# Kernel tuning notes

Measured on AMD Instinct MI355X. Metric: run time of the kernel, lower is better.

Reference implementation:

```python
import jax, jax.numpy as jnp
import numpy as np

B, H, W, DIM = 1, 256, 256, 192
HEADS = 6
K, DIL = 7, 2            # NAttention kernel / dilation
WS, DF = 8, 2            # stripe window size, anchor down factor
AWS = WS // DF           # anchor window size (4)
N1, N2 = WS * WS, AWS * AWS
L = H * W
CPB_HID = 512


def _nbr(size, k, d):
    # 1D neighborhood-attention neighbor indices with dilation (edge-clamped)
    i = np.arange(size); g = i % d; p = i // d
    gsize = size // d  # d divides size
    start = np.clip(p - k // 2, 0, gsize - k)
    nbr_p = start[:, None] + np.arange(k)[None, :]
    nbr = g[:, None] + d * nbr_p                    # absolute key index
    rb = nbr_p - p[:, None] + (k - 1)               # rpb index in [0, 2k-2]
    return nbr.astype(np.int32), rb.astype(np.int32)

NBR_H, RB_H = _nbr(H, K, DIL)
NBR_W, RB_W = _nbr(W, K, DIL)


def _na_attention(q, k, v, rpb):
    # q,k,v: (B, heads, H, W, hd); rpb: (heads, 2K-1, 2K-1)
    bias = rpb[:, RB_H, :]                          # (heads,H,K,2K-1)
    bias = jnp.take(bias, RB_W, axis=3)             # (heads,H,K,W,K)
    bias = jnp.transpose(bias, (0, 1, 3, 2, 4))     # (heads,H,W,K,K)
    logits = []
    for ki in range(K):
        kh = jnp.take(k, NBR_H[:, ki], axis=2)
        for kj in range(K):
            khw = jnp.take(kh, NBR_W[:, kj], axis=3)
            logits.append(jnp.einsum('bnhwc,bnhwc->bnhw', q, khw))
    a = jnp.stack(logits, axis=-1).reshape(*q.shape[:4], K, K) + bias[None]
    a = jax.nn.softmax(a.reshape(*q.shape[:4], K * K), axis=-1).reshape(*q.shape[:4], K, K)
    out = jnp.zeros_like(q)
    for ki in range(K):
        vh = jnp.take(v, NBR_H[:, ki], axis=2)
        for kj in range(K):
            vhw = jnp.take(vh, NBR_W[:, kj], axis=3)
            out = out + a[..., ki, kj, None] * vhw
    return out

na_attention = jax.checkpoint(_na_attention)


def window_partition(x, ws):
    b, h, w, c = x.shape
    x = x.reshape(b, h // ws, ws, w // ws, ws, c)
    return jnp.transpose(x, (0, 1, 3, 2, 4, 5)).reshape(-1, ws * ws, c)


def window_reverse(x, ws, h, w):
    c = x.shape[-1]
    b = x.shape[0] // ((h // ws) * (w // ws))
    x = x.reshape(b, h // ws, w // ws, ws, ws, c)
    return jnp.transpose(x, (0, 1, 3, 2, 4, 5)).reshape(b, h, w, c)


def _l2n(x):
    n = jnp.linalg.norm(x, axis=-1, keepdims=True)
    return x / jnp.maximum(n, 1e-12)


def _affine(attn, table, index, ls, w1, b1, w2):
    # attn: (Bw, heads, Na, Nb)
    attn = attn * jnp.exp(jnp.minimum(ls, float(np.log(100.0))))[None]
    bt = jax.nn.relu(table.reshape(-1, 2) @ w1 + b1) @ w2           # (T, heads)
    bias = bt[index.reshape(-1)].reshape(index.shape[0], index.shape[1], HEADS)
    bias = 16.0 * jax.nn.sigmoid(jnp.transpose(bias, (2, 0, 1)))    # (heads,Na,Nb)
    return attn + bias[None]


def _cos_attn(q, k, v, table, index, ls, w1, b1, w2):
    attn = jnp.einsum('bhnc,bhmc->bhnm', _l2n(q), _l2n(k))
    attn = jax.nn.softmax(_affine(attn, table, index, ls, w1, b1, w2), axis=-1)
    return attn @ v


def _forward(x, h_size, w_size, table, index_a2w, index_w2a, qkv_w, qkv_b,
             anchor_dw_w, anchor_dw_b, anchor_pw_w, anchor_pw_b,
             na_qkv_w, na_qkv_b, na_after_w, na_after_b, na_rpb,
             ls1, cpb1_w1, cpb1_b1, cpb1_w2, ls2, cpb2_w1, cpb2_b1, cpb2_w2,
             proj_w, proj_b):
    Bx, Lx, C = x.shape
    Hs, Ws_ = int(h_size), int(w_size)
    qkv = x @ qkv_w + qkv_b                     # (B,L,3C)
    half = C * 3 // 2
    qkv_window, qkv_stripe = qkv[..., :half], qkv[..., half:]
    # anchor projection: depthwise conv (k=DF+1, stride=DF) + pointwise
    xi = x.reshape(Bx, Hs, Ws_, C)
    a = jax.lax.conv_general_dilated(
        xi, anchor_dw_w, (DF, DF), ((1, 1), (1, 1)),
        dimension_numbers=('NHWC', 'HWIO', 'NHWC'), feature_group_count=C) + anchor_dw_b
    a = a @ anchor_pw_w + anchor_pw_b           # (B, H/DF, W/DF, C//2)
    # ---- neighborhood attention branch ----
    hd = C // HEADS
    xw = qkv_window.reshape(Bx, Hs, Ws_, half)
    q2 = (xw @ na_qkv_w + na_qkv_b).reshape(Bx, Hs, Ws_, 3, HEADS, hd)
    q2 = jnp.transpose(q2, (3, 0, 4, 1, 2, 5))  # (3,B,heads,H,W,hd)
    qn, kn, vn = q2[0] * hd ** -0.5, q2[1], q2[2]
    xna = na_attention(qn, kn, vn, na_rpb)
    xna = jnp.transpose(xna, (0, 2, 3, 1, 4)).reshape(Bx, Hs, Ws_, C)
    xna = (xna @ na_after_w + na_after_b).reshape(Bx, Lx, C // 2)
    # ---- anchor stripe attention branch ----
    qs = window_partition(qkv_stripe.reshape(Bx, Hs, Ws_, half), WS)  # (Bw,N1,1.5C)
    an = window_partition(a, AWS)                                     # (Bw,N2,C//2)
    Bw = qs.shape[0]
    hs = C // 2 // HEADS
    q3 = jnp.transpose(qs.reshape(Bw, N1, 3, HEADS, hs), (2, 0, 3, 1, 4))
    q_s, k_s, v_s = q3[0], q3[1], q3[2]
    an = jnp.transpose(an.reshape(Bw, N2, HEADS, hs), (0, 2, 1, 3))
    x1 = _cos_attn(an, k_s, v_s, table, index_a2w, ls1, cpb1_w1, cpb1_b1, cpb1_w2)
    x2 = _cos_attn(q_s, an, x1, table, index_w2a, ls2, cpb2_w1, cpb2_b1, cpb2_w2)
    x2 = jnp.transpose(x2, (0, 2, 1, 3)).reshape(Bw, N1, C // 2)
    xs = window_reverse(x2, WS, Hs, Ws_).reshape(Bx, Lx, C // 2)
    return jnp.concatenate([xna, xs], axis=-1) @ proj_w + proj_b


def setup_inputs() -> dict:
    key = jax.random.key(0)
    ks = jax.random.split(key, 16)
    f = lambda i, shp, s=0.02: jax.random.normal(ks[i], shp, dtype=jnp.float32) * s
    x = jax.random.normal(ks[0], (B, L, DIM), dtype=jnp.float32)
    # swin-v2 style normalized log-spaced relative coords table
    rc = np.arange(-(WS - 1), WS, dtype=np.float32) / (WS - 1)
    t = np.stack(np.meshgrid(rc, rc, indexing='ij'), axis=-1)[None]
    table = jnp.asarray(np.sign(t) * np.log2(1 + np.abs(t) * 8) / 3.0, dtype=jnp.float32)
    wc = np.arange(WS); ac = np.arange(AWS) * DF
    cw = np.stack(np.meshgrid(wc, wc, indexing='ij'), -1).reshape(-1, 2)
    ca = np.stack(np.meshgrid(ac, ac, indexing='ij'), -1).reshape(-1, 2)
    def _idx(c1, c2):
        d = c1[:, None, :] - c2[None, :, :]
        return jnp.asarray((d[..., 0] + WS - 1) * (2 * WS - 1) + (d[..., 1] + WS - 1), dtype=jnp.int32)
    return {
        'x': x, 'h_size': H, 'w_size': W, 'table': table,
        'index_a2w': _idx(ca, cw), 'index_w2a': _idx(cw, ca),
        'qkv_w': f(1, (DIM, 3 * DIM)), 'qkv_b': jnp.zeros((3 * DIM,), jnp.float32),
        'anchor_dw_w': f(2, (DF + 1, DF + 1, 1, DIM), 0.1),
        'anchor_dw_b': jnp.zeros((DIM,), jnp.float32),
        'anchor_pw_w': f(3, (DIM, DIM // 2)), 'anchor_pw_b': jnp.zeros((DIM // 2,), jnp.float32),
        'na_qkv_w': f(4, (3 * DIM // 2, 3 * DIM)), 'na_qkv_b': jnp.zeros((3 * DIM,), jnp.float32),
        'na_after_w': f(5, (DIM, DIM // 2)), 'na_after_b': jnp.zeros((DIM // 2,), jnp.float32),
        'na_rpb': f(6, (HEADS, 2 * K - 1, 2 * K - 1)),
        'ls1': jnp.log(10.0) * jnp.ones((HEADS, 1, 1), jnp.float32),
        'cpb1_w1': f(7, (2, CPB_HID), 0.1), 'cpb1_b1': jnp.zeros((CPB_HID,), jnp.float32),
        'cpb1_w2': f(8, (CPB_HID, HEADS), 0.1),
        'ls2': jnp.log(10.0) * jnp.ones((HEADS, 1, 1), jnp.float32),
        'cpb2_w1': f(9, (2, CPB_HID), 0.1), 'cpb2_b1': jnp.zeros((CPB_HID,), jnp.float32),
        'cpb2_w2': f(10, (CPB_HID, HEADS), 0.1),
        'proj_w': f(11, (DIM, DIM)), 'proj_b': jnp.zeros((DIM,), jnp.float32),
    }


def reference(x, h_size, w_size, table, index_a2w, index_w2a, qkv_w, qkv_b,
              anchor_dw_w, anchor_dw_b, anchor_pw_w, anchor_pw_b,
              na_qkv_w, na_qkv_b, na_after_w, na_after_b, na_rpb,
              ls1, cpb1_w1, cpb1_b1, cpb1_w2, ls2, cpb2_w1, cpb2_b1, cpb2_w2,
              proj_w, proj_b):
    return _forward(x, h_size, w_size, table, index_a2w, index_w2a, qkv_w, qkv_b,
                    anchor_dw_w, anchor_dw_b, anchor_pw_w, anchor_pw_b,
                    na_qkv_w, na_qkv_b, na_after_w, na_after_b, na_rpb,
                    ls1, cpb1_w1, cpb1_b1, cpb1_w2, ls2, cpb2_w1, cpb2_b1, cpb2_w2,
                    proj_w, proj_b)
```

## Files before the change

kernel.cpp:

```cpp
#include <hip/hip_runtime.h>
#include <math.h>


typedef unsigned short bf16_t;
typedef __attribute__((ext_vector_type(8))) short short8;
typedef __attribute__((ext_vector_type(4))) float f32x4;

__device__ inline float bf2f(bf16_t v) { return __uint_as_float((unsigned)v << 16); }
__device__ inline bf16_t f2bf(float f) {
    unsigned u = __float_as_uint(f);
    unsigned r = (u + 0x7fffu + ((u >> 16) & 1u)) >> 16;
    return (bf16_t)r;
}
__device__ inline float cvt(float v) { return v; }
__device__ inline float cvt(bf16_t v) { return bf2f(v); }
__device__ inline void sto(float* p, float v) { *p = v; }
__device__ inline void sto(bf16_t* p, float v) { *p = f2bf(v); }

__device__ inline void ld_bf8(const bf16_t* p, float* d) {
    uint4 r = *(const uint4*)p;
    d[0] = __uint_as_float(r.x << 16); d[1] = __uint_as_float(r.x & 0xffff0000u);
    d[2] = __uint_as_float(r.y << 16); d[3] = __uint_as_float(r.y & 0xffff0000u);
    d[4] = __uint_as_float(r.z << 16); d[5] = __uint_as_float(r.z & 0xffff0000u);
    d[6] = __uint_as_float(r.w << 16); d[7] = __uint_as_float(r.w & 0xffff0000u);
}
__device__ inline unsigned pk2(float a, float b) {
    return (unsigned)f2bf(a) | ((unsigned)f2bf(b) << 16);
}

template <int KD, int NA, int NCOL, typename TO>
__global__ __launch_bounds__(256) void mfma_gemm_k(
    const bf16_t* __restrict__ A, const bf16_t* __restrict__ Bt,
    const float* __restrict__ bias, TO* __restrict__ C,
    int lda, int ldb, int ldc)
{
    const int bid  = blockIdx.x;
    const int work = (bid & 7) * (gridDim.x >> 3) + (bid >> 3);
    const int brow = work / NCOL;
    const int bcol = work - brow * NCOL;

    const int t = threadIdx.x;
    const int lane = t & 63, wave = t >> 6;
    const int wr = wave >> 1, wc = wave & 1;
    const int m0 = brow * 128 + wr * 64;
    const int n0 = bcol * 96 + wc * 48;
    const int lm = lane & 15;
    const int q  = lane >> 4;

    f32x4 acc[4][3] = {};
    const bf16_t* ap = A + (size_t)(m0 + lm) * lda + q * 8;
    const bf16_t* bp = Bt + (size_t)(n0 + lm) * ldb + q * 8;

#pragma unroll
    for (int k0 = 0; k0 < KD; k0 += 32) {
        short8 af[4], bf[3];
#pragma unroll
        for (int mi = 0; mi < 4; mi++)
            af[mi] = *(const short8*)(ap + (size_t)(mi * 16) * lda + k0);
#pragma unroll
        for (int ni = 0; ni < 3; ni++)
            bf[ni] = *(const short8*)(bp + (size_t)(ni * 16) * ldb + k0);
#pragma unroll
        for (int mi = 0; mi < 4; mi++)
#pragma unroll
            for (int ni = 0; ni < 3; ni++)
                acc[mi][ni] = __builtin_amdgcn_mfma_f32_16x16x32_bf16(
                    af[mi], bf[ni], acc[mi][ni], 0, 0, 0);
    }

#pragma unroll
    for (int mi = 0; mi < 4; mi++) {
#pragma unroll
        for (int ni = 0; ni < 3; ni++) {
            int col = n0 + ni * 16 + lm;
            float bv = bias[col];
            if (NA) {
                int which = col / 192;
                int hh = (col % 192) / 32;
                int d  = col % 32;
                size_t pbase = ((size_t)which * 6 + hh) * 2097152 + d;
#pragma unroll
                for (int r = 0; r < 4; r++) {
                    int row = m0 + mi * 16 + q * 4 + r;
                    int ii = row >> 8, jj = row & 255;
                    int par = ((ii & 1) << 1) | (jj & 1);
                    int pixin = (ii >> 1) * 128 + (jj >> 1);
                    sto(&C[pbase + ((size_t)(par * 16384 + pixin) << 5)],
                        acc[mi][ni][r] + bv);
                }
            } else {
#pragma unroll
                for (int r = 0; r < 4; r++) {
                    int row = m0 + mi * 16 + q * 4 + r;
                    sto(&C[(size_t)row * ldc + col], acc[mi][ni][r] + bv);
                }
            }
        }
    }
}

__global__ __launch_bounds__(256) void vtpose_k(
    const bf16_t* __restrict__ nap, bf16_t* __restrict__ vt)
{
    __shared__ unsigned short tl[32][144];
    const int b = blockIdx.x;
    const int z = b >> 7;
    const int tile = b & 127;
    const int h = z >> 2, par = z & 3;
    const int pix0 = tile << 7;

    const bf16_t* sp = nap + (size_t)(12 + h) * 2097152
                     + ((size_t)(par * 16384 + pix0) << 5);
    const int t = threadIdx.x;
    {
        const int px = t & 127, half = t >> 7;
        uint4 r0 = *(const uint4*)(sp + px * 32 + half * 16);
        uint4 r1 = *(const uint4*)(sp + px * 32 + half * 16 + 8);
        const unsigned short* u0 = (const unsigned short*)&r0;
        const unsigned short* u1 = (const unsigned short*)&r1;
#pragma unroll
        for (int i = 0; i < 8; i++) tl[half * 16 + i][px] = u0[i];
#pragma unroll
        for (int i = 0; i < 8; i++) tl[half * 16 + 8 + i][px] = u1[i];
    }
    __syncthreads();
    {
        const int d = t >> 3, g = t & 7;
        unsigned short buf[16];
#pragma unroll
        for (int i = 0; i < 16; i++) buf[i] = tl[d][g * 16 + i];
        bf16_t* dp = vt + ((size_t)z << 19) + ((size_t)d << 14) + pix0 + g * 16;
        *(uint4*)dp = *(uint4*)buf;
        *(uint4*)(dp + 8) = *(uint4*)(buf + 8);
    }
}

__global__ __launch_bounds__(256) void cvt_bf16_k(
    const float* __restrict__ src, bf16_t* __restrict__ dst, int n8)
{
    int tid = blockIdx.x * 256 + threadIdx.x;
    if (tid >= n8) return;
    float4 a = ((const float4*)src)[tid * 2];
    float4 b = ((const float4*)src)[tid * 2 + 1];
    uint4 o;
    o.x = pk2(a.x, a.y); o.y = pk2(a.z, a.w);
    o.z = pk2(b.x, b.y); o.w = pk2(b.z, b.w);
    ((uint4*)dst)[tid] = o;
}

__global__ __launch_bounds__(256) void tcvt_k(
    const float* __restrict__ W, bf16_t* __restrict__ Wt,
    int Kd, int N, int ld, int coloff)
{
    int tid = blockIdx.x * 256 + threadIdx.x;
    if (tid >= Kd * N) return;
    int k = tid % Kd, n = tid / Kd;
    Wt[tid] = f2bf(W[(size_t)k * ld + coloff + n]);
}

__global__ __launch_bounds__(256) void tpose_qkvw_k(
    const float* __restrict__ W, float* __restrict__ WT)
{
    int tid = blockIdx.x * 256 + threadIdx.x;
    if (tid >= 288 * 192) return;
    int k = tid % 192, j = tid / 192;
    WT[tid] = W[(size_t)k * 576 + j];
}

__global__ __launch_bounds__(256) void fold_wna_t_k(
    const float* __restrict__ qkv_wT, const float* __restrict__ na_qkv_w,
    bf16_t* __restrict__ Wna_t)
{
    int tid = blockIdx.x * 256 + threadIdx.x;
    if (tid >= 576 * 192) return;
    int k = tid % 192, n = tid / 192;
    float acc = 0.f;
    for (int j = 0; j < 288; j++)
        acc += qkv_wT[j * 192 + k] * na_qkv_w[j * 576 + n];
    Wna_t[tid] = f2bf(acc);
}

__global__ __launch_bounds__(256) void fold_bna_k(
    const float* __restrict__ qkv_b, const float* __restrict__ na_qkv_w,
    const float* __restrict__ na_qkv_b, float* __restrict__ bna)
{
    int j = blockIdx.x * 256 + threadIdx.x;
    if (j >= 576) return;
    float acc = na_qkv_b[j];
    for (int k = 0; k < 288; k++)
        acc += qkv_b[k] * na_qkv_w[k * 576 + j];
    bna[j] = acc;
}

__global__ __launch_bounds__(256) void cpb_k(
    const float* __restrict__ table, const float* __restrict__ w1,
    const float* __restrict__ b1, const float* __restrict__ w2,
    float* __restrict__ bt)
{
    int tid = blockIdx.x * 256 + threadIdx.x;
    if (tid >= 225 * 6) return;
    int h = tid % 6, t = tid / 6;
    float t0 = table[t * 2], t1 = table[t * 2 + 1];
    float acc = 0.f;
    for (int m = 0; m < 512; m++) {
        float hv = t0 * w1[m] + t1 * w1[512 + m] + b1[m];
        hv = fmaxf(hv, 0.f);
        acc += hv * w2[m * 6 + h];
    }
    bt[tid] = acc;
}

__global__ __launch_bounds__(256) void sigb_k(
    const float* __restrict__ bt, const int* __restrict__ idx,
    float* __restrict__ bp)
{
    int tid = blockIdx.x * 256 + threadIdx.x;
    if (tid >= 6144) return;
    int h = tid >> 10, p = tid & 1023;
    bp[tid] = 16.0f / (1.0f + __expf(-bt[idx[p] * 6 + h]));
}

__global__ __launch_bounds__(256) void sigb1T_k(
    const float* __restrict__ bt, const int* __restrict__ idx,
    float* __restrict__ bp)
{
    int tid = blockIdx.x * 256 + threadIdx.x;
    if (tid >= 6144) return;
    int h = tid >> 10, p = tid & 1023;
    int m = p >> 4, n2 = p & 15;
    bp[tid] = 16.0f / (1.0f + __expf(-bt[idx[n2 * 64 + m] * 6 + h]));
}

#define BM 64
#define BN 64
#define BKK 16
template <typename TA, typename TO>
__global__ __launch_bounds__(256) void gemm_k(
    const TA* __restrict__ A, const float* __restrict__ B,
    const float* __restrict__ bias, TO* __restrict__ C,
    int M, int N, int Kd, int lda, int ldb, int ldc)
{
    __shared__ float As[BKK][BM + 1];
    __shared__ float Bs[BKK][BN + 1];
    const int t  = threadIdx.x;
    const int tx = t & 15, ty = t >> 4;
    const int m0 = blockIdx.y * BM, n0 = blockIdx.x * BN;
    float acc[4][4] = {};

    for (int k0 = 0; k0 < Kd; k0 += BKK) {
#pragma unroll
        for (int i = 0; i < 4; i++) {
            int m = (t >> 4) + i * 16;
            int k = t & 15;
            int gm = m0 + m, gk = k0 + k;
            As[k][m] = (gm < M && gk < Kd) ? cvt(A[(size_t)gm * lda + gk]) : 0.f;
        }
#pragma unroll
        for (int i = 0; i < 4; i++) {
            int k = (t >> 6) + i * 4;
            int n = t & 63;
            int gk = k0 + k, gn = n0 + n;
            Bs[k][n] = (gk < Kd && gn < N) ? B[(size_t)gk * ldb + gn] : 0.f;
        }
        __syncthreads();
#pragma unroll
        for (int k = 0; k < BKK; k++) {
            float a[4], b[4];
#pragma unroll
            for (int i = 0; i < 4; i++) a[i] = As[k][ty * 4 + i];
#pragma unroll
            for (int j = 0; j < 4; j++) b[j] = Bs[k][tx * 4 + j];
#pragma unroll
            for (int i = 0; i < 4; i++)
#pragma unroll
                for (int j = 0; j < 4; j++) acc[i][j] += a[i] * b[j];
        }
        __syncthreads();
    }
#pragma unroll
    for (int i = 0; i < 4; i++) {
        int gm = m0 + ty * 4 + i;
        if (gm >= M) continue;
#pragma unroll
        for (int j = 0; j < 4; j++) {
            int gn = n0 + tx * 4 + j;
            if (gn >= N) continue;
            sto(&C[(size_t)gm * ldc + gn], acc[i][j] + bias[gn]);
        }
    }
}

__global__ __launch_bounds__(256) void dwconv_k(
    const float* __restrict__ x, const float* __restrict__ w,
    const float* __restrict__ b, float* __restrict__ adw)
{
    int tid = blockIdx.x * 256 + threadIdx.x;
    if (tid >= 16384 * 48) return;
    int c4 = tid % 48;
    int p = tid / 48;
    int ow = p & 127, oh = p >> 7;
    int c = c4 * 4;
    float4 s = *(const float4*)(b + c);
#pragma unroll
    for (int kh = 0; kh < 3; kh++) {
        int ih = oh * 2 - 1 + kh;
        if (ih < 0 || ih >= 256) continue;
#pragma unroll
        for (int kw = 0; kw < 3; kw++) {
            int iw = ow * 2 - 1 + kw;
            if (iw < 0 || iw >= 256) continue;
            float4 xv = *(const float4*)(x + (size_t)(ih * 256 + iw) * 192 + c);
            float4 wv = *(const float4*)(w + (kh * 3 + kw) * 192 + c);
            s.x += xv.x * wv.x; s.y += xv.y * wv.y;
            s.z += xv.z * wv.z; s.w += xv.w * wv.w;
        }
    }
    *(float4*)(adw + (size_t)p * 192 + c) = s;
}

__global__ __launch_bounds__(256) void na_attn_k(
    const bf16_t* __restrict__ nap, const bf16_t* __restrict__ vt,
    const float* __restrict__ rpb, bf16_t* __restrict__ outp)
{
    __shared__ float rpb_s[176];
    __shared__ __align__(16) unsigned P_s[4][16][20];

    const int bid  = blockIdx.x;
    const int work = (bid & 7) * 768 + (bid >> 3);
    const int z    = work >> 8;
    const int rem  = work & 255;
    const int pi   = rem >> 1;
    const int xh   = rem & 1;

    const int t = threadIdx.x;
    const int wv = t >> 6, lane = t & 63;
    const int lm = lane & 15, lq = lane >> 4;
    const int h = z >> 2, par = z & 3;

    if (t < 169) rpb_s[t] = rpb[h * 169 + t];
    __syncthreads();

    const int pj0 = xh * 64 + wv * 16;
    const int si  = min(max(pi - 3, 0), 121);
    const int rbh0 = si - pi + 6;
    const int c0  = min(max(pj0 - 3, 0), 121) & ~7;

    const size_t plane = (size_t)65536 * 32;
    const size_t poff  = (size_t)(par * 16384) * 32;
    const bf16_t* qpl = nap + (size_t)h * plane + poff;
    const bf16_t* kpl = nap + (size_t)(6 + h) * plane + poff;
    const bf16_t* vtpl = vt + ((size_t)z << 19);

    const short8 qf = *(const short8*)(qpl + ((size_t)(pi * 128 + pj0 + lm)) * 32 + lq * 8);

    int offc[4][2]; bool vm[4][2];
#pragma unroll
    for (int r = 0; r < 4; r++) {
        int q = lq * 4 + r, pj = pj0 + q;
        int sj = min(max(pj - 3, 0), 121);
#pragma unroll
        for (int t2 = 0; t2 < 2; t2++) {
            int c = c0 + 2 * lm + t2;
            vm[r][t2] = (c >= sj) && (c <= sj + 6);
            offc[r][t2] = min(max(c - pj + 6, 0), 12);
        }
    }
    const int kc0 = min(c0 + 2 * lm,     127) * 64;
    const int kc1 = min(c0 + 2 * lm + 1, 127) * 64;
    const int vcol = c0 + (lq << 3);
    const size_t vb0 = (size_t)lm * 16384;
    const size_t vb1 = (size_t)(lm + 16) * 16384;

    const float scale = 0.17677669529663687f;
    f32x4 o0 = {}, o1 = {};
    float sums[4] = {0.f, 0.f, 0.f, 0.f};
    const f32x4 zz = {};

#pragma unroll 2
    for (int rr = 0; rr < 7; rr++) {
        const char* krow = (const char*)kpl + (size_t)((si + rr) * 128) * 64;

        short8 kf0 = *(const short8*)(krow + kc0 + lq * 16);
        short8 kf1 = *(const short8*)(krow + kc1 + lq * 16);
        f32x4 s0 = __builtin_amdgcn_mfma_f32_16x16x32_bf16(qf, kf0, zz, 0, 0, 0);
        f32x4 s1 = __builtin_amdgcn_mfma_f32_16x16x32_bf16(qf, kf1, zz, 0, 0, 0);

        const float* br = rpb_s + (rbh0 + rr) * 13;
        float e0[4], e1[4];
#pragma unroll
        for (int r = 0; r < 4; r++) {
            float a0 = __expf(fmaf(s0[r], scale, br[offc[r][0]]));
            float a1 = __expf(fmaf(s1[r], scale, br[offc[r][1]]));
            a0 = vm[r][0] ? a0 : 0.f;
            a1 = vm[r][1] ? a1 : 0.f;
            e0[r] = a0; e1[r] = a1;
            sums[r] += a0 + a1;
        }
#pragma unroll
        for (int r = 0; r < 4; r++) {
            unsigned pr;
            asm("v_cvt_pk_bf16_f32 %0, %1, %2" : "=v"(pr) : "v"(e0[r]), "v"(e1[r]));
            P_s[wv][lq * 4 + r][lm] = pr;
        }
        const short8 pf = *(const short8*)((const bf16_t*)P_s[wv][lm] + lq * 8);

        int rowo = min((si + rr) * 128 + vcol, 16376);
        short8 vf0 = *(const short8*)(vtpl + vb0 + rowo);
        short8 vf1 = *(const short8*)(vtpl + vb1 + rowo);

        o0 = __builtin_amdgcn_mfma_f32_16x16x32_bf16(pf, vf0, o0, 0, 0, 0);
        o1 = __builtin_amdgcn_mfma_f32_16x16x32_bf16(pf, vf1, o1, 0, 0, 0);
    }

#pragma unroll
    for (int r = 0; r < 4; r++) {
        float s = sums[r];
        s += __shfl_xor(s, 1, 64);
        s += __shfl_xor(s, 2, 64);
        s += __shfl_xor(s, 4, 64);
        s += __shfl_xor(s, 8, 64);
        sums[r] = 1.0f / s;
    }

    const int gi = par >> 1, gj = par & 1;
    const int i0 = pi * 2 + gi;
    bf16_t* ob = outp + ((size_t)i0 * 256 + gj) * 192 + h * 32 + lm;
#pragma unroll
    for (int r = 0; r < 4; r++) {
        int q = lq * 4 + r;
        size_t px = (size_t)(pj0 + q) * 2 * 192;
        ob[px]      = f2bf(o0[r] * sums[r]);
        ob[px + 16] = f2bf(o1[r] * sums[r]);
    }
}

__global__ __launch_bounds__(256) void attn1_k(
    const float* __restrict__ apw,
    const bf16_t* __restrict__ qkvs,
    const float* __restrict__ b1pT,
    const float* __restrict__ ls1,
    float* __restrict__ x1)
{
    __shared__ float bT_s[1024];
    __shared__ __align__(16) unsigned P_s[4][16][36];

    const int t = threadIdx.x;
    const int wv = t >> 6, lane = t & 63;
    const int lm = lane & 15, lq = lane >> 4;
    const int h = blockIdx.y;
    const int w = blockIdx.x * 4 + wv;
    const int wi = w >> 5, wj = w & 31;

#pragma unroll
    for (int i = 0; i < 4; i++) bT_s[i * 256 + t] = b1pT[h * 1024 + i * 256 + t];
    __syncthreads();

    const float scale = __expf(fminf(ls1[h], 4.605170185988091f));

    short8 af = {};
    float an2 = 0.f;
    {
        int ay = wi * 4 + (lm >> 2), ax = wj * 4 + (lm & 3);
        const float* ap = apw + (size_t)(ay * 128 + ax) * 96 + h * 16;
        if (lq < 2) {
            float4 v0 = *(const float4*)(ap + lq * 8);
            float4 v1 = *(const float4*)(ap + lq * 8 + 4);
            float vs[8] = {v0.x, v0.y, v0.z, v0.w, v1.x, v1.y, v1.z, v1.w};
            unsigned* au = (unsigned*)&af;
#pragma unroll
            for (int j2 = 0; j2 < 4; j2++) {
                unsigned u = pk2(vs[2 * j2], vs[2 * j2 + 1]);
                au[j2] = u;
                float lo = __uint_as_float(u << 16);
                float hi = __uint_as_float(u & 0xffff0000u);
                an2 += lo * lo + hi * hi;
            }
        }
    }
    an2 += __shfl_xor(an2, 16, 64);
    an2 += __shfl_xor(an2, 32, 64);
    const float sa = scale / fmaxf(sqrtf(an2), 1e-12f);

    const f32x4 zz = {};
    f32x4 o = {};
    float sum = 0.f;

#pragma unroll
    for (int g = 0; g < 2; g++) {
#pragma unroll
        for (int tt = 0; tt < 2; tt++) {
            const int tile = g * 2 + tt;
            int py = wi * 8 + tile * 2 + (lm >> 3);
            int px = wj * 8 + (lm & 7);
            const bf16_t* kp = qkvs + (size_t)(py * 256 + px) * 288 + 96 + h * 16;
            short8 kf = {};
            float kn2 = 0.f;
            float klo[4], khi[4];
            if (lq < 2) {
                uint4 kr = *(const uint4*)(kp + lq * 8);
                unsigned ku[4] = {kr.x, kr.y, kr.z, kr.w};
#pragma unroll
                for (int j2 = 0; j2 < 4; j2++) {
                    klo[j2] = __uint_as_float(ku[j2] << 16);
                    khi[j2] = __uint_as_float(ku[j2] & 0xffff0000u);
                    kn2 += klo[j2] * klo[j2] + khi[j2] * khi[j2];
                }
            }
            kn2 += __shfl_xor(kn2, 16, 64);
            kn2 += __shfl_xor(kn2, 32, 64);
            float rk = 1.0f / fmaxf(sqrtf(kn2), 1e-12f);
            if (lq < 2) {
                unsigned* kuo = (unsigned*)&kf;
#pragma unroll
                for (int j2 = 0; j2 < 4; j2++)
                    kuo[j2] = pk2(klo[j2] * rk, khi[j2] * rk);
            }
            f32x4 s = __builtin_amdgcn_mfma_f32_16x16x32_bf16(kf, af, zz, 0, 0, 0);
            float e[4];
#pragma unroll
            for (int r = 0; r < 4; r++) {
                e[r] = __expf(fmaf(s[r], sa,
                              bT_s[((tile * 16 + lq * 4 + r) << 4) + lm]));
                sum += e[r];
            }
            P_s[wv][lm][tile * 8 + lq * 2]     = pk2(e[0], e[1]);
            P_s[wv][lm][tile * 8 + lq * 2 + 1] = pk2(e[2], e[3]);
        }
        const short8 pf = *(const short8*)&P_s[wv][lm][g * 16 + lq * 4];
        short8 vf;
        int pyv = wi * 8 + g * 4 + lq;
        const bf16_t* vrow = qkvs + (size_t)(pyv * 256 + wj * 8) * 288 + 192 + h * 16 + lm;
#pragma unroll
        for (int i = 0; i < 8; i++)
            ((bf16_t*)&vf)[i] = vrow[(size_t)i * 288];
        o = __builtin_amdgcn_mfma_f32_16x16x32_bf16(pf, vf, o, 0, 0, 0);
    }

    sum += __shfl_xor(sum, 16, 64);
    sum += __shfl_xor(sum, 32, 64);
    const float inv = 1.0f / sum;
    float* xp = x1 + ((size_t)w * 6 + h) * 256;
#pragma unroll
    for (int r = 0; r < 4; r++) {
        float iv = __shfl(inv, lq * 4 + r, 64);
        xp[(lq * 4 + r) * 16 + lm] = o[r] * iv;
    }
}

__global__ __launch_bounds__(256) void attn2_k(
    const float* __restrict__ apw,
    const bf16_t* __restrict__ qkvs,
    const float* __restrict__ b2p,
    const float* __restrict__ ls2,
    const float* __restrict__ x1,
    bf16_t* __restrict__ cat)
{
    int tid = blockIdx.x * 256 + threadIdx.x;
    if (tid >= 1024 * 6 * 64) return;
    int n1 = tid & 63;
    int h = (tid >> 6) % 6;
    int w = tid / 384;
    int wi = w >> 5, wj = w & 31;
    float scale = __expf(fminf(ls2[h], 4.605170185988091f));

    int qy = wi * 8 + (n1 >> 3), qx = wj * 8 + (n1 & 7);
    const bf16_t* qp = qkvs + (size_t)(qy * 256 + qx) * 288 + h * 16;
    float qv[16];
    ld_bf8(qp, qv); ld_bf8(qp + 8, qv + 8);
    float nrm = 0.f;
#pragma unroll
    for (int d = 0; d < 16; d++) nrm += qv[d] * qv[d];
    float innorm = 1.0f / fmaxf(sqrtf(nrm), 1e-12f);
#pragma unroll
    for (int d = 0; d < 16; d++) qv[d] *= innorm;

    const float* bp = b2p + h * 1024 + n1 * 16;
    float sum = 0.f;
    float acc[16] = {};
#pragma unroll
    for (int m = 0; m < 16; m++) {
        int ay = wi * 4 + (m >> 2), ax = wj * 4 + (m & 3);
        const float* ap = apw + (size_t)(ay * 128 + ax) * 96 + h * 16;
        float dot = 0.f, kn = 0.f;
#pragma unroll
        for (int d = 0; d < 16; d += 4) {
            float4 v = *(const float4*)(ap + d);
            dot += qv[d] * v.x + qv[d + 1] * v.y + qv[d + 2] * v.z + qv[d + 3] * v.w;
            kn += v.x * v.x + v.y * v.y + v.z * v.z + v.w * v.w;
        }
        dot *= 1.0f / fmaxf(sqrtf(kn), 1e-12f);
        float e = __expf(fmaf(dot, scale, bp[m]));
        sum += e;
        const float* vp = x1 + ((size_t)w * 6 + h) * 256 + m * 16;
#pragma unroll
        for (int d = 0; d < 16; d += 4) {
            float4 v = *(const float4*)(vp + d);
            acc[d] += e * v.x; acc[d + 1] += e * v.y;
            acc[d + 2] += e * v.z; acc[d + 3] += e * v.w;
        }
    }
    float inv = 1.0f / sum;
#pragma unroll
    for (int d = 0; d < 16; d++) acc[d] *= inv;
    bf16_t* op = cat + (size_t)(qy * 256 + qx) * 192 + 96 + h * 16;
    uint4 o0, o1;
    o0.x = pk2(acc[0], acc[1]);   o0.y = pk2(acc[2], acc[3]);
    o0.z = pk2(acc[4], acc[5]);   o0.w = pk2(acc[6], acc[7]);
    o1.x = pk2(acc[8], acc[9]);   o1.y = pk2(acc[10], acc[11]);
    o1.z = pk2(acc[12], acc[13]); o1.w = pk2(acc[14], acc[15]);
    *(uint4*)(op) = o0;
    *(uint4*)(op + 8) = o1;
}

extern "C" void kernel_launch(void* const* d_in, const int* in_sizes, int n_in,
                              void* d_out, int out_size, void* d_ws, size_t ws_size,
                              hipStream_t stream) {
    const float* x          = (const float*)d_in[0];
    const float* table      = (const float*)d_in[3];
    const int*   idx_a2w    = (const int*)d_in[4];
    const int*   idx_w2a    = (const int*)d_in[5];
    const float* qkv_w      = (const float*)d_in[6];
    const float* qkv_b      = (const float*)d_in[7];
    const float* adw_w      = (const float*)d_in[8];
    const float* adw_b      = (const float*)d_in[9];
    const float* apw_w      = (const float*)d_in[10];
    const float* apw_b      = (const float*)d_in[11];
    const float* na_qkv_w   = (const float*)d_in[12];
    const float* na_qkv_b   = (const float*)d_in[13];
    const float* na_after_w = (const float*)d_in[14];
    const float* na_after_b = (const float*)d_in[15];
    const float* na_rpb     = (const float*)d_in[16];
    const float* ls1        = (const float*)d_in[17];
    const float* cpb1_w1    = (const float*)d_in[18];
    const float* cpb1_b1    = (const float*)d_in[19];
    const float* cpb1_w2    = (const float*)d_in[20];
    const float* ls2        = (const float*)d_in[21];
    const float* cpb2_w1    = (const float*)d_in[22];
    const float* cpb2_b1    = (const float*)d_in[23];
    const float* cpb2_w2    = (const float*)d_in[24];
    const float* proj_w     = (const float*)d_in[25];
    const float* proj_b     = (const float*)d_in[26];
    float* out = (float*)d_out;
    (void)in_sizes; (void)n_in; (void)out_size; (void)ws_size;

    char* base = (char*)d_ws;
    size_t off = 0;
    auto alloc = [&](size_t bytes) {
        off = (off + 255) & ~(size_t)255;
        void* p = base + off; off += bytes; return p;
    };
    float*  bna    = (float*)alloc(576 * 4);
    float*  bt1    = (float*)alloc(225 * 6 * 4);
    float*  bt2    = (float*)alloc(225 * 6 * 4);
    float*  b1pT   = (float*)alloc(6144 * 4);
    float*  b2p    = (float*)alloc(6144 * 4);
    float*  qkv_wT = (float*)alloc(288 * 192 * 4);
    bf16_t* Wna_t  = (bf16_t*)alloc(576 * 192 * 2);
    bf16_t* Ws_t   = (bf16_t*)alloc(288 * 192 * 2);
    bf16_t* Waft_t = (bf16_t*)alloc(96 * 192 * 2);
    bf16_t* Wproj_t= (bf16_t*)alloc(192 * 192 * 2);
    bf16_t* qkvs   = (bf16_t*)alloc((size_t)65536 * 288 * 2);
    char*   naR    = (char*)alloc((size_t)65536 * 576 * 2);
    char*   R      = (char*)alloc((size_t)65536 * 192 * 2);
    float*  apw    = (float*)alloc((size_t)16384 * 96 * 4);
    bf16_t* naqkv   = (bf16_t*)naR;
    float*  x1      = (float*)naR;
    bf16_t* cat     = (bf16_t*)(naR + (8 << 20));
    bf16_t* xb      = (bf16_t*)R;
    float*  adw     = (float*)R;
    bf16_t* xna_pre = (bf16_t*)R;
    bf16_t* vt      = (bf16_t*)out;

    tpose_qkvw_k<<<216, 256, 0, stream>>>(qkv_w, qkv_wT);
    fold_wna_t_k<<<432, 256, 0, stream>>>(qkv_wT, na_qkv_w, Wna_t);
    fold_bna_k<<<3, 256, 0, stream>>>(qkv_b, na_qkv_w, na_qkv_b, bna);
    cpb_k<<<6, 256, 0, stream>>>(table, cpb1_w1, cpb1_b1, cpb1_w2, bt1);
    cpb_k<<<6, 256, 0, stream>>>(table, cpb2_w1, cpb2_b1, cpb2_w2, bt2);
    sigb1T_k<<<24, 256, 0, stream>>>(bt1, idx_a2w, b1pT);
    sigb_k<<<24, 256, 0, stream>>>(bt2, idx_w2a, b2p);
    tcvt_k<<<216, 256, 0, stream>>>(qkv_w, Ws_t, 192, 288, 576, 288);
    tcvt_k<<<72, 256, 0, stream>>>(na_after_w, Waft_t, 192, 96, 96, 0);
    tcvt_k<<<144, 256, 0, stream>>>(proj_w, Wproj_t, 192, 192, 192, 0);
    cvt_bf16_k<<<6144, 256, 0, stream>>>(x, xb, 65536 * 192 / 8);

    mfma_gemm_k<192, 0, 3, bf16_t><<<1536, 256, 0, stream>>>(
        xb, Ws_t, qkv_b + 288, qkvs, 192, 192, 288);

    mfma_gemm_k<192, 1, 6, bf16_t><<<3072, 256, 0, stream>>>(
        xb, Wna_t, bna, naqkv, 192, 192, 576);

    vtpose_k<<<3072, 256, 0, stream>>>(naqkv, vt);

    dwconv_k<<<3072, 256, 0, stream>>>(x, adw_w, adw_b, adw);
    gemm_k<float, float><<<dim3(2, 256), 256, 0, stream>>>(
        adw, apw_w, apw_b, apw, 16384, 96, 192, 192, 96, 96);

    na_attn_k<<<6144, 256, 0, stream>>>(naqkv, vt, na_rpb, xna_pre);

    mfma_gemm_k<192, 0, 1, bf16_t><<<512, 256, 0, stream>>>(
        xna_pre, Waft_t, na_after_b, cat, 192, 192, 192);

    attn1_k<<<dim3(256, 6), 256, 0, stream>>>(apw, qkvs, b1pT, ls1, x1);
    attn2_k<<<1536, 256, 0, stream>>>(apw, qkvs, b2p, ls2, x1, cat);

    mfma_gemm_k<192, 0, 2, float><<<1024, 256, 0, stream>>>(
        cat, Wproj_t, proj_b, out, 192, 192, 192);
}
```

Before: 613.8 us.

## Split NA attention loop into batched QK, softmax, and PV phases

Restructures the neighborhood-attention kernel's per-row loop into three fully unrolled phases. All seven QK MFMAs are issued first, then exp/bias is computed and written into a larger per-wave shared P buffer, then the PV MFMAs run into two alternating accumulator pairs. The goal is to expose more independent MFMA and memory work and to break the serial accumulator dependency. In exchange it raises register pressure (28 score floats) and grows LDS use per block about sevenfold, which may cut occupancy.

```diff
diff --git a/kernel.cpp b/kernel.cpp
--- a/kernel.cpp
+++ b/kernel.cpp
@@ -323,7 +323,7 @@
     const float* __restrict__ rpb, bf16_t* __restrict__ outp)
 {
     __shared__ float rpb_s[176];
-    __shared__ __align__(16) unsigned P_s[4][16][20];
+    __shared__ __align__(16) unsigned P_s[4][16][140];
 
     const int bid  = blockIdx.x;
     const int work = (bid & 7) * 768 + (bid >> 3);
@@ -372,54 +372,60 @@
     const size_t vb1 = (size_t)(lm + 16) * 16384;
 
     const float scale = 0.17677669529663687f;
-    f32x4 o0 = {}, o1 = {};
-    float sums[4] = {0.f, 0.f, 0.f, 0.f};
     const f32x4 zz = {};
 
-#pragma unroll 2
+    f32x4 s[7][2];
+#pragma unroll
     for (int rr = 0; rr < 7; rr++) {
         const char* krow = (const char*)kpl + (size_t)((si + rr) * 128) * 64;
-
         short8 kf0 = *(const short8*)(krow + kc0 + lq * 16);
         short8 kf1 = *(const short8*)(krow + kc1 + lq * 16);
-        f32x4 s0 = __builtin_amdgcn_mfma_f32_16x16x32_bf16(qf, kf0, zz, 0, 0, 0);
-        f32x4 s1 = __builtin_amdgcn_mfma_f32_16x16x32_bf16(qf, kf1, zz, 0, 0, 0);
-
+        s[rr][0] = __builtin_amdgcn_mfma_f32_16x16x32_bf16(qf, kf0, zz, 0, 0, 0);
+        s[rr][1] = __builtin_amdgcn_mfma_f32_16x16x32_bf16(qf, kf1, zz, 0, 0, 0);
+    }
+
+    float sums[4] = {0.f, 0.f, 0.f, 0.f};
+#pragma unroll
+    for (int rr = 0; rr < 7; rr++) {
         const float* br = rpb_s + (rbh0 + rr) * 13;
-        float e0[4], e1[4];
 #pragma unroll
         for (int r = 0; r < 4; r++) {
-            float a0 = __expf(fmaf(s0[r], scale, br[offc[r][0]]));
-            float a1 = __expf(fmaf(s1[r], scale, br[offc[r][1]]));
+            float a0 = __expf(fmaf(s[rr][0][r], scale, br[offc[r][0]]));
+            float a1 = __expf(fmaf(s[rr][1][r], scale, br[offc[r][1]]));
             a0 = vm[r][0] ? a0 : 0.f;
             a1 = vm[r][1] ? a1 : 0.f;
-            e0[r] = a0; e1[r] = a1;
             sums[r] += a0 + a1;
-        }
-#pragma unroll
-        for (int r = 0; r < 4; r++) {
             unsigned pr;
-            asm("v_cvt_pk_bf16_f32 %0, %1, %2" : "=v"(pr) : "v"(e0[r]), "v"(e1[r]));
-            P_s[wv][lq * 4 + r][lm] = pr;
-        }
-        const short8 pf = *(const short8*)((const bf16_t*)P_s[wv][lm] + lq * 8);
-
+            asm("v_cvt_pk_bf16_f32 %0, %1, %2" : "=v"(pr) : "v"(a0), "v"(a1));
+            P_s[wv][lq * 4 + r][rr * 20 + lm] = pr;
+        }
+    }
+
+    f32x4 o0a = {}, o0b = {}, o1a = {}, o1b = {};
+#pragma unroll
+    for (int rr = 0; rr < 7; rr++) {
+        const short8 pf = *(const short8*)&P_s[wv][lm][rr * 20 + lq * 4];
         int rowo = min((si + rr) * 128 + vcol, 16376);
         short8 vf0 = *(const short8*)(vtpl + vb0 + rowo);
         short8 vf1 = *(const short8*)(vtpl + vb1 + rowo);
-
-        o0 = __builtin_amdgcn_mfma_f32_16x16x32_bf16(pf, vf0, o0, 0, 0, 0);
-        o1 = __builtin_amdgcn_mfma_f32_16x16x32_bf16(pf, vf1, o1, 0, 0, 0);
-    }
+        if (rr & 1) {
+            o0b = __builtin_amdgcn_mfma_f32_16x16x32_bf16(pf, vf0, o0b, 0, 0, 0);
+            o1b = __builtin_amdgcn_mfma_f32_16x16x32_bf16(pf, vf1, o1b, 0, 0, 0);
+        } else {
+            o0a = __builtin_amdgcn_mfma_f32_16x16x32_bf16(pf, vf0, o0a, 0, 0, 0);
+            o1a = __builtin_amdgcn_mfma_f32_16x16x32_bf16(pf, vf1, o1a, 0, 0, 0);
+        }
+    }
+    f32x4 o0 = o0a + o0b, o1 = o1a + o1b;
 
 #pragma unroll
     for (int r = 0; r < 4; r++) {
-        float s = sums[r];
-        s += __shfl_xor(s, 1, 64);
-        s += __shfl_xor(s, 2, 64);
-        s += __shfl_xor(s, 4, 64);
-        s += __shfl_xor(s, 8, 64);
-        sums[r] = 1.0f / s;
+        float sm = sums[r];
+        sm += __shfl_xor(sm, 1, 64);
+        sm += __shfl_xor(sm, 2, 64);
+        sm += __shfl_xor(sm, 4, 64);
+        sm += __shfl_xor(sm, 8, 64);
+        sums[r] = 1.0f / sm;
     }
 
     const int gi = par >> 1, gj = par & 1;
```

After: 621.5 us. About the same (+1.3%).

## Fuse V transpose into NA qkv GEMM epilogue via LDS-staged coalesced stores

Applied to the files above, without the earlier changes.

The NA qkv GEMM epilogue now stages the output tile in shared memory and writes Q/K in parity-split layout with 16-byte coalesced stores. The V part is written directly in transposed (d-major) layout, so the separate vtpose kernel and its extra read/write of V are removed. The neighborhood attention row loop is also fully unrolled. The cost is extra LDS use and a barrier per GEMM block, plus strided LDS reads for the V transpose. The V half no longer writes its non-transposed copy to naqkv, so this assumes attention only reads V from vt.

```diff
diff --git a/kernel.cpp b/kernel.cpp
--- a/kernel.cpp
+++ b/kernel.cpp
@@ -32,8 +32,11 @@
 __global__ __launch_bounds__(256) void mfma_gemm_k(
     const bf16_t* __restrict__ A, const bf16_t* __restrict__ Bt,
     const float* __restrict__ bias, TO* __restrict__ C,
+    bf16_t* __restrict__ C2,
     int lda, int ldb, int ldc)
 {
+    __shared__ bf16_t Cs[NA ? 128 : 1][NA ? 104 : 1];
+
     const int bid  = blockIdx.x;
     const int work = (bid & 7) * (gridDim.x >> 3) + (bid >> 3);
     const int brow = work / NCOL;
@@ -68,27 +71,69 @@
                     af[mi], bf[ni], acc[mi][ni], 0, 0, 0);
     }
 
-#pragma unroll
-    for (int mi = 0; mi < 4; mi++) {
-#pragma unroll
-        for (int ni = 0; ni < 3; ni++) {
-            int col = n0 + ni * 16 + lm;
-            float bv = bias[col];
-            if (NA) {
-                int which = col / 192;
-                int hh = (col % 192) / 32;
-                int d  = col % 32;
-                size_t pbase = ((size_t)which * 6 + hh) * 2097152 + d;
+    if (NA) {
+#pragma unroll
+        for (int mi = 0; mi < 4; mi++) {
+#pragma unroll
+            for (int ni = 0; ni < 3; ni++) {
+                int lcol = wc * 48 + ni * 16 + lm;
+                float bv = bias[bcol * 96 + lcol];
 #pragma unroll
                 for (int r = 0; r < 4; r++) {
-                    int row = m0 + mi * 16 + q * 4 + r;
-                    int ii = row >> 8, jj = row & 255;
-                    int par = ((ii & 1) << 1) | (jj & 1);
-                    int pixin = (ii >> 1) * 128 + (jj >> 1);
-                    sto(&C[pbase + ((size_t)(par * 16384 + pixin) << 5)],
-                        acc[mi][ni][r] + bv);
+                    int lrow = wr * 64 + mi * 16 + q * 4 + r;
+                    Cs[lrow][lcol] = f2bf(acc[mi][ni][r] + bv);
                 }
-            } else {
+            }
+        }
+        __syncthreads();
+
+        const int which = bcol >> 1;
+        const int hh0   = (bcol & 1) * 3;
+        const int gi    = (brow >> 1) & 1;
+        const int pixbase = (brow >> 2) * 128 + (brow & 1) * 64;
+
+        if (which < 2) {
+            const int px = t >> 2, d8 = (t & 3) << 3;
+#pragma unroll
+            for (int hh_l = 0; hh_l < 3; hh_l++) {
+#pragma unroll
+                for (int gj = 0; gj < 2; gj++) {
+                    int par = gi * 2 + gj;
+                    bf16_t* dst = (bf16_t*)C
+                        + (size_t)(which * 6 + hh0 + hh_l) * 2097152
+                        + ((size_t)(par * 16384 + pixbase) << 5);
+                    uint4 v = *(const uint4*)&Cs[2 * px + gj][hh_l * 32 + d8];
+                    *(uint4*)(dst + px * 32 + d8) = v;
+                }
+            }
+        } else {
+#pragma unroll
+            for (int rd = 0; rd < 6; rd++) {
+                int task = rd * 256 + t;
+                int seg  = task >> 3;
+                int px8  = (task & 7) << 3;
+                int hh_l = seg / 64;
+                int rem  = seg - hh_l * 64;
+                int d    = rem >> 1;
+                int gj   = rem & 1;
+                int par  = gi * 2 + gj;
+                unsigned short buf[8];
+#pragma unroll
+                for (int i = 0; i < 8; i++)
+                    buf[i] = Cs[2 * (px8 + i) + gj][hh_l * 32 + d];
+                bf16_t* dst = C2
+                    + (((size_t)(hh0 + hh_l) * 4 + par) << 19)
+                    + ((size_t)d << 14) + pixbase + px8;
+                *(uint4*)dst = *(uint4*)buf;
+            }
+        }
+    } else {
+#pragma unroll
+        for (int mi = 0; mi < 4; mi++) {
+#pragma unroll
+            for (int ni = 0; ni < 3; ni++) {
+                int col = n0 + ni * 16 + lm;
+                float bv = bias[col];
 #pragma unroll
                 for (int r = 0; r < 4; r++) {
                     int row = m0 + mi * 16 + q * 4 + r;
@@ -96,42 +141,6 @@
                 }
             }
         }
-    }
-}
-
-__global__ __launch_bounds__(256) void vtpose_k(
-    const bf16_t* __restrict__ nap, bf16_t* __restrict__ vt)
-{
-    __shared__ unsigned short tl[32][144];
-    const int b = blockIdx.x;
-    const int z = b >> 7;
-    const int tile = b & 127;
-    const int h = z >> 2, par = z & 3;
-    const int pix0 = tile << 7;
-
-    const bf16_t* sp = nap + (size_t)(12 + h) * 2097152
-                     + ((size_t)(par * 16384 + pix0) << 5);
-    const int t = threadIdx.x;
-    {
-        const int px = t & 127, half = t >> 7;
-        uint4 r0 = *(const uint4*)(sp + px * 32 + half * 16);
-        uint4 r1 = *(const uint4*)(sp + px * 32 + half * 16 + 8);
-        const unsigned short* u0 = (const unsigned short*)&r0;
-        const unsigned short* u1 = (const unsigned short*)&r1;
-#pragma unroll
-        for (int i = 0; i < 8; i++) tl[half * 16 + i][px] = u0[i];
-#pragma unroll
-        for (int i = 0; i < 8; i++) tl[half * 16 + 8 + i][px] = u1[i];
-    }
-    __syncthreads();
-    {
-        const int d = t >> 3, g = t & 7;
-        unsigned short buf[16];
-#pragma unroll
-        for (int i = 0; i < 16; i++) buf[i] = tl[d][g * 16 + i];
-        bf16_t* dp = vt + ((size_t)z << 19) + ((size_t)d << 14) + pix0 + g * 16;
-        *(uint4*)dp = *(uint4*)buf;
-        *(uint4*)(dp + 8) = *(uint4*)(buf + 8);
     }
 }
 
@@ -376,7 +385,7 @@
     float sums[4] = {0.f, 0.f, 0.f, 0.f};
     const f32x4 zz = {};
 
-#pragma unroll 2
+#pragma unroll
     for (int rr = 0; rr < 7; rr++) {
         const char* krow = (const char*)kpl + (size_t)((si + rr) * 128) * 64;
 
@@ -684,12 +693,10 @@
     cvt_bf16_k<<<6144, 256, 0, stream>>>(x, xb, 65536 * 192 / 8);
 
     mfma_gemm_k<192, 0, 3, bf16_t><<<1536, 256, 0, stream>>>(
-        xb, Ws_t, qkv_b + 288, qkvs, 192, 192, 288);
+        xb, Ws_t, qkv_b + 288, qkvs, nullptr, 192, 192, 288);
 
     mfma_gemm_k<192, 1, 6, bf16_t><<<3072, 256, 0, stream>>>(
-        xb, Wna_t, bna, naqkv, 192, 192, 576);
-
-    vtpose_k<<<3072, 256, 0, stream>>>(naqkv, vt);
+        xb, Wna_t, bna, naqkv, vt, 192, 192, 576);
 
     dwconv_k<<<3072, 256, 0, stream>>>(x, adw_w, adw_b, adw);
     gemm_k<float, float><<<dim3(2, 256), 256, 0, stream>>>(
@@ -698,11 +705,11 @@
     na_attn_k<<<6144, 256, 0, stream>>>(naqkv, vt, na_rpb, xna_pre);
 
     mfma_gemm_k<192, 0, 1, bf16_t><<<512, 256, 0, stream>>>(
-        xna_pre, Waft_t, na_after_b, cat, 192, 192, 192);
+        xna_pre, Waft_t, na_after_b, cat, nullptr, 192, 192, 192);
 
     attn1_k<<<dim3(256, 6), 256, 0, stream>>>(apw, qkvs, b1pT, ls1, x1);
     attn2_k<<<1536, 256, 0, stream>>>(apw, qkvs, b2p, ls2, x1, cat);
 
     mfma_gemm_k<192, 0, 2, float><<<1024, 256, 0, stream>>>(
-        cat, Wproj_t, proj_b, out, 192, 192, 192);
-}
+        cat, Wproj_t, proj_b, out, nullptr, 192, 192, 192);
+}
```

New measurement: 576.4 us. 6.1% less time.
